# Kernel optimization log

Hardware: AMD Instinct MI355X
Metric: run time of the kernel (lower is better)

## Reference

```python
import jax, jax.numpy as jnp
import numpy as np

# dims: B batch, S seq, IN input, H lstm hidden, OUT output, N memory_size, W memory_width
B, S, IN, H, OUT, N, W = 128, 32, 512, 1024, 512, 16384, 128
C = OUT + W + (2 * W + 3)  # controller_output_size = 899


def setup_inputs() -> dict:
    key = jax.random.key(0)
    ks = jax.random.split(key, 16)
    def p(k, shape, s=0.02):
        return jax.random.normal(k, shape, jnp.float32) * s
    return {
        'x': jax.random.normal(ks[0], (B, S, IN), jnp.float32),
        'memory': p(ks[1], (N, W), 0.1),
        'Wih': p(ks[2], (4 * H, IN + W)), 'Whh': p(ks[3], (4 * H, H)),
        'bih': jnp.zeros(4 * H, jnp.float32), 'bhh': jnp.zeros(4 * H, jnp.float32),
        'Wout': p(ks[4], (C, H)), 'bout': jnp.zeros(C, jnp.float32),
        'rkW': p(ks[5], (W, C)), 'rkb': jnp.zeros(W, jnp.float32),
        'rbW': p(ks[6], (1, C)), 'rbb': jnp.zeros(1, jnp.float32),
        'rgW': p(ks[7], (1, C)), 'rgb': jnp.zeros(1, jnp.float32),
        'wkW': p(ks[8], (W, C)), 'wkb': jnp.zeros(W, jnp.float32),
        'wbW': p(ks[9], (1, C)), 'wbb': jnp.zeros(1, jnp.float32),
        'wgW': p(ks[10], (1, C)), 'wgb': jnp.zeros(1, jnp.float32),
        'erW': p(ks[11], (W, C)), 'erb': jnp.zeros(W, jnp.float32),
        'adW': p(ks[12], (W, C)), 'adb': jnp.zeros(W, jnp.float32),
        'pW': p(ks[13], (OUT, OUT)), 'pb': jnp.zeros(OUT, jnp.float32),
    }


def _l2norm(v, axis):
    n = jnp.linalg.norm(v, axis=axis, keepdims=True)
    return v / jnp.maximum(n, 1e-12)


def reference(x, memory, Wih, Whh, bih, bhh, Wout, bout,
              rkW, rkb, rbW, rbb, rgW, rgb,
              wkW, wkb, wbW, wbb, wgW, wgb,
              erW, erb, adW, adb, pW, pb):
    Bq, Sq, _ = x.shape
    Nq, Wq = memory.shape
    Hq = Whh.shape[1]
    out_size = pW.shape[0]
    sp = jax.nn.softplus
    uniform = jnp.full((Bq, Nq), 1.0 / Nq, x.dtype)

    def addressing(keyv, beta, gamma, prev_w, mem):
        # cosine similarity -> softmax(beta*sim) -> interpolation with prev weights
        sim = _l2norm(keyv, 1) @ _l2norm(mem, 1).T        # [B, N]
        w = jax.nn.softmax(beta * sim, axis=1)
        return gamma * w + (1 - gamma) * prev_w

    def step(carry, xt):
        mem, h, c, prev_rw, prev_rv = carry
        ci = jnp.concatenate([xt, prev_rv], axis=1)       # [B, IN+W]
        g = ci @ Wih.T + h @ Whh.T + bih + bhh
        i_, f_, gg, o_ = jnp.split(g, 4, axis=1)          # torch LSTM gate order i,f,g,o
        c = jax.nn.sigmoid(f_) * c + jax.nn.sigmoid(i_) * jnp.tanh(gg)
        h = jax.nn.sigmoid(o_) * jnp.tanh(c)
        co = h @ Wout.T + bout                            # controller output [B, C]
        # read head
        rkey = co @ rkW.T + rkb
        rbeta = sp(co @ rbW.T + rbb)
        rgamma = 1 + sp(co @ rgW.T + rgb)
        rw = addressing(rkey, rbeta, rgamma, prev_rw, mem)
        # write head (prev weights = uniform, per source)
        wkey = co @ wkW.T + wkb
        wbeta = sp(co @ wbW.T + wbb)
        wgamma = 1 + sp(co @ wgW.T + wgb)
        ww = addressing(wkey, wbeta, wgamma, uniform, mem)
        er = jax.nn.sigmoid(co @ erW.T + erb)             # [B, W]
        ad = jnp.tanh(co @ adW.T + adb)                   # [B, W]
        # MemoryBank.write sums erase/add terms over batch (shared global memory)
        erase = jnp.einsum('bn,bw->nw', ww, er)
        addt = jnp.einsum('bn,bw->nw', ww, ad)
        mem = mem * (1 - erase) + addt
        rv = rw @ mem                                     # read after write [B, W]
        out = co[:, :out_size] @ pW.T + pb
        return (mem, h, c, rw, rv), out

    init = (memory,
            jnp.zeros((Bq, Hq), x.dtype), jnp.zeros((Bq, Hq), x.dtype),
            uniform, jnp.zeros((Bq, Wq), x.dtype))
    _, outs = jax.lax.scan(step, init, jnp.swapaxes(x, 0, 1))
    return jnp.swapaxes(outs, 0, 1)                       # [B, S, OUT]
```

## Files before the change

### kernel.cpp

```cpp
#include <hip/hip_runtime.h>

typedef __attribute__((ext_vector_type(8))) short bf16x8;
typedef __attribute__((ext_vector_type(4))) float f32x4;

__device__ __forceinline__ float bf2f(unsigned short u) {
  union { float f; unsigned int i; } v; v.i = ((unsigned int)u) << 16; return v.f;
}
__device__ __forceinline__ unsigned short f2bf(float f) {
  union { float f; unsigned int i; } v; v.f = f;
  unsigned int r = v.i + 0x7fffu + ((v.i >> 16) & 1u);
  return (unsigned short)(r >> 16);
}
__device__ __forceinline__ float sigf(float x) { return 1.0f / (1.0f + expf(-x)); }
__device__ __forceinline__ float softplusf(float x) {
  return (x > 20.0f) ? x : log1pf(expf(x));
}
__device__ __forceinline__ float sat(float v) {
  return fminf(fmaxf(v, -1.0e6f), 1.0e6f);
}
__device__ __forceinline__ float ldx(const void* p, int is32, long i) {
  return is32 ? ((const float*)p)[i] : bf2f(((const unsigned short*)p)[i]);
}
template<int A32>
__device__ __forceinline__ bf16x8 load8(const void* base, long off) {
  if (A32) {
    const float* p = (const float*)base + off;
    f32x4 a = *(const f32x4*)p;
    f32x4 b = *(const f32x4*)(p + 4);
    bf16x8 r;
    r[0] = (short)f2bf(a[0]); r[1] = (short)f2bf(a[1]);
    r[2] = (short)f2bf(a[2]); r[3] = (short)f2bf(a[3]);
    r[4] = (short)f2bf(b[0]); r[5] = (short)f2bf(b[1]);
    r[6] = (short)f2bf(b[2]); r[7] = (short)f2bf(b[3]);
    return r;
  }
  return *(const bf16x8*)((const unsigned short*)base + off);
}


__global__ __launch_bounds__(64) void probe_dtype(
    const unsigned int* __restrict__ w, int* __restrict__ flags)
{
  const int lane = threadIdx.x;
  int cnt = 0;
  for (int i = 0; i < 16; ++i) {
    unsigned int word = w[lane * 16 + i];
    float av = fabsf(bf2f((unsigned short)(word & 0xFFFFu)));
    if (av > 1.0e-4f && av < 1.0f) cnt++;
  }
  #pragma unroll
  for (int off = 32; off > 0; off >>= 1) cnt += __shfl_xor(cnt, off);
  if (lane == 0) flags[1] = (cnt > 512) ? 0 : 1;
}

__global__ __launch_bounds__(64) void probe_layout(int* __restrict__ flags) {
  const int lane = threadIdx.x;
  const int qr = lane & 15, quad = lane >> 4;
  bf16x8 a, b;
  #pragma unroll
  for (int j = 0; j < 8; ++j) {
    int k = quad * 8 + j;
    a[j] = (short)f2bf((k == qr) ? 1.0f : 0.0f);
    b[j] = (short)f2bf((float)(k + 1));
  }
  f32x4 acc = {0.0f, 0.0f, 0.0f, 0.0f};
  acc = __builtin_amdgcn_mfma_f32_16x16x32_bf16(a, b, acc, 0, 0, 0);
  bool ok0 = true, ok1 = true;
  #pragma unroll
  for (int rg = 0; rg < 4; ++rg) {
    ok0 = ok0 && (acc[rg] == (float)(quad * 4 + rg + 1));
    ok1 = ok1 && (acc[rg] == (float)(qr + 1));
  }
  int a0 = __all(ok0 ? 1 : 0);
  int a1 = __all(ok1 ? 1 : 0);
  if (lane == 0) flags[0] = a0 ? 0 : (a1 ? 1 : 0);
}

template<int BM, int BN, int EPI, int A32, int BT>
__global__ __launch_bounds__(256) void gemm_pipe(
    const void* __restrict__ A, int lda,
    const unsigned short* __restrict__ B, int ldb,
    int kChunk, int Mtot, int Ntot,
    float* __restrict__ C, long long ldc, unsigned short* __restrict__ Cb,
    const int* __restrict__ flags)
{
  constexpr int LDT = 72;
  constexpr int AI = BM / 32;
  constexpr int BI = BN / 32;
  __shared__ unsigned short smem[2][(BM + BN) * LDT];
  const int tid = threadIdx.x;
  const int lane = tid & 63, wid = tid >> 6;
  const int wm = wid & 1, wn = wid >> 1;
  constexpr int WM = BM / 2, WN = BN / 2;
  constexpr int TM = WM / 16, TN = WN / 16;
  const int m0 = blockIdx.x * BM, n0 = blockIdx.y * BN;
  const int kBeg = blockIdx.z * kChunk;
  const int qr = lane & 15, quad = lane >> 4;
  const int NIT = kChunk >> 6;

  f32x4 acc[TM][TN] = {};
  bf16x8 ar[AI], br[BI];

  auto loadAB = [&](int k0) {
    #pragma unroll
    for (int i = 0; i < AI; ++i) {
      int lin = i * 256 + tid; int row = lin >> 3, q = (lin & 7) << 3;
      ar[i] = load8<A32>(A, (long)(m0 + row) * lda + k0 + q);
    }
    #pragma unroll
    for (int i = 0; i < BI; ++i) {
      int lin = i * 256 + tid;
      if (BT) {
        int kl = lin >> 3, nq = (lin & 7) << 3;
        br[i] = *(const bf16x8*)(B + (long)(k0 + kl) * ldb + n0 + nq);
      } else {
        int row = lin >> 3, q = (lin & 7) << 3;
        br[i] = *(const bf16x8*)(B + (long)(n0 + row) * ldb + k0 + q);
      }
    }
  };
  auto stage = [&](int buf) {
    #pragma unroll
    for (int i = 0; i < AI; ++i) {
      int lin = i * 256 + tid; int row = lin >> 3, q = (lin & 7) << 3;
      *(bf16x8*)&smem[buf][row * LDT + q] = ar[i];
    }
    #pragma unroll
    for (int i = 0; i < BI; ++i) {
      int lin = i * 256 + tid;
      if (BT) {
        int kl = lin >> 3, nq = (lin & 7) << 3;
        #pragma unroll
        for (int j = 0; j < 8; ++j)
          smem[buf][(BM + nq + j) * LDT + kl] = (unsigned short)br[i][j];
      } else {
        int row = lin >> 3, q = (lin & 7) << 3;
        *(bf16x8*)&smem[buf][(BM + row) * LDT + q] = br[i];
      }
    }
  };

  loadAB(kBeg);
  stage(0);
  __syncthreads();
  for (int it = 0; it < NIT; ++it) {
    if (it + 1 < NIT) loadAB(kBeg + (it + 1) * 64);
    const unsigned short* As = &smem[it & 1][0];
    const unsigned short* Bs = &smem[it & 1][BM * LDT];
    #pragma unroll
    for (int ks = 0; ks < 64; ks += 32) {
      bf16x8 af[TM], bfv[TN];
      #pragma unroll
      for (int mt = 0; mt < TM; ++mt)
        af[mt] = *(const bf16x8*)&As[(wm * WM + mt * 16 + qr) * LDT + ks + quad * 8];
      #pragma unroll
      for (int nt = 0; nt < TN; ++nt)
        bfv[nt] = *(const bf16x8*)&Bs[(wn * WN + nt * 16 + qr) * LDT + ks + quad * 8];
      #pragma unroll
      for (int mt = 0; mt < TM; ++mt)
        #pragma unroll
        for (int nt = 0; nt < TN; ++nt)
          acc[mt][nt] = __builtin_amdgcn_mfma_f32_16x16x32_bf16(af[mt], bfv[nt], acc[mt][nt], 0, 0, 0);
    }
    if (it + 1 < NIT) { stage((it + 1) & 1); __syncthreads(); }
  }

  const int swap = flags[0];
  #pragma unroll
  for (int mt = 0; mt < TM; ++mt)
    #pragma unroll
    for (int nt = 0; nt < TN; ++nt)
      #pragma unroll
      for (int rg = 0; rg < 4; ++rg) {
        int ri = swap ? qr : (quad * 4 + rg);
        int ci = swap ? (quad * 4 + rg) : qr;
        int gm = m0 + wm * WM + mt * 16 + ri;
        int gn = n0 + wn * WN + nt * 16 + ci;
        float v = sat(acc[mt][nt][rg]);
        if (EPI == 2) Cb[(size_t)gm * ldc + gn] = f2bf(v);
        else C[(size_t)blockIdx.z * Mtot * Ntot + (size_t)gm * Ntot + gn] = v;
      }
}

__global__ __launch_bounds__(256) void gemm_gates(
    const unsigned short* __restrict__ A, const unsigned short* __restrict__ B,
    const float* __restrict__ bsum2, float* __restrict__ c,
    unsigned short* __restrict__ nxt, const unsigned short* __restrict__ x_bf,
    int t, const int* __restrict__ flags)
{
  constexpr int LDT = 72;
  __shared__ unsigned short smem[2][128 * LDT];
  __shared__ float Ssc[64][65];
  const int tid = threadIdx.x;
  const int lane = tid & 63, wid = tid >> 6;
  const int wm = wid & 1, wn = wid >> 1;
  const int m0 = blockIdx.x * 64, n0 = blockIdx.y * 64;
  const int qr = lane & 15, quad = lane >> 4;
  const int NIT = 26;

  f32x4 acc[2][2] = {};
  bf16x8 ar[2], br[2];
  auto loadAB = [&](int k0) {
    #pragma unroll
    for (int i = 0; i < 2; ++i) {
      int lin = i * 256 + tid; int row = lin >> 3, q = (lin & 7) << 3;
      ar[i] = *(const bf16x8*)(A + (long)(m0 + row) * 1664 + k0 + q);
      br[i] = *(const bf16x8*)(B + (long)(n0 + row) * 1664 + k0 + q);
    }
  };
  auto stage = [&](int buf) {
    #pragma unroll
    for (int i = 0; i < 2; ++i) {
      int lin = i * 256 + tid; int row = lin >> 3, q = (lin & 7) << 3;
      *(bf16x8*)&smem[buf][row * LDT + q] = ar[i];
      *(bf16x8*)&smem[buf][(64 + row) * LDT + q] = br[i];
    }
  };
  loadAB(0); stage(0); __syncthreads();
  for (int it = 0; it < NIT; ++it) {
    if (it + 1 < NIT) loadAB((it + 1) * 64);
    const unsigned short* As = &smem[it & 1][0];
    const unsigned short* Bs = &smem[it & 1][64 * LDT];
    #pragma unroll
    for (int ks = 0; ks < 64; ks += 32) {
      bf16x8 af[2], bfv[2];
      #pragma unroll
      for (int mt = 0; mt < 2; ++mt)
        af[mt] = *(const bf16x8*)&As[(wm * 32 + mt * 16 + qr) * LDT + ks + quad * 8];
      #pragma unroll
      for (int nt = 0; nt < 2; ++nt)
        bfv[nt] = *(const bf16x8*)&Bs[(wn * 32 + nt * 16 + qr) * LDT + ks + quad * 8];
      #pragma unroll
      for (int mt = 0; mt < 2; ++mt)
        #pragma unroll
        for (int nt = 0; nt < 2; ++nt)
          acc[mt][nt] = __builtin_amdgcn_mfma_f32_16x16x32_bf16(af[mt], bfv[nt], acc[mt][nt], 0, 0, 0);
    }
    if (it + 1 < NIT) { stage((it + 1) & 1); __syncthreads(); }
  }

  const int swap = flags[0];
  #pragma unroll
  for (int mt = 0; mt < 2; ++mt)
    #pragma unroll
    for (int nt = 0; nt < 2; ++nt)
      #pragma unroll
      for (int rg = 0; rg < 4; ++rg) {
        int ri = swap ? qr : (quad * 4 + rg);
        int ci = swap ? (quad * 4 + rg) : qr;
        Ssc[wn * 32 + nt * 16 + ci][wm * 32 + mt * 16 + ri] = acc[mt][nt][rg];
      }
  __syncthreads();
  {
    const int jl = tid & 15, bh = tid >> 4;
    const int jg = (n0 >> 2) + jl;
    const float b0 = bsum2[n0 + jl * 4 + 0];
    const float b1 = bsum2[n0 + jl * 4 + 1];
    const float b2 = bsum2[n0 + jl * 4 + 2];
    const float b3 = bsum2[n0 + jl * 4 + 3];
    #pragma unroll
    for (int p = 0; p < 4; ++p) {
      int bl = bh + p * 16;
      int bb = m0 + bl;
      float gi_ = Ssc[jl * 4 + 0][bl] + b0;
      float gf  = Ssc[jl * 4 + 1][bl] + b1;
      float gg  = Ssc[jl * 4 + 2][bl] + b2;
      float go  = Ssc[jl * 4 + 3][bl] + b3;
      size_t cix = (size_t)bb * 1024 + jg;
      float cn = sat(sigf(gf) * c[cix] + sigf(gi_) * tanhf(gg));
      c[cix] = cn;
      nxt[bb * 1664 + 640 + jg] = f2bf(sigf(go) * tanhf(cn));
    }
  }
  if (t + 1 < 32) {
    int blk = blockIdx.y * 2 + blockIdx.x;
    #pragma unroll
    for (int i = 0; i < 2; ++i) {
      int e = blk * 512 + i * 256 + tid;
      nxt[(e >> 9) * 1664 + (e & 511)] = x_bf[(size_t)(t + 1) * 65536 + e];
    }
  }
}

__global__ __launch_bounds__(256) void gemm_heads(
    const unsigned short* __restrict__ Wcomb,
    const unsigned short* __restrict__ h, int ldb,
    const float* __restrict__ vcat,
    unsigned short* __restrict__ keys_n, unsigned short* __restrict__ EA,
    float* __restrict__ sc, void* __restrict__ outp, int t,
    const int* __restrict__ flags)
{
  constexpr int BM = 128, BN = 64, LDT = 72;
  __shared__ unsigned short smem[2][(BM + BN) * LDT];
  __shared__ float colss[64];
  __shared__ float cinv[64];
  const int tid = threadIdx.x;
  const int lane = tid & 63, wid = tid >> 6;
  const int wm = wid & 1, wn = wid >> 1;
  constexpr int TM = 4, TN = 2;
  const int m0 = blockIdx.x * BM, n0 = blockIdx.y * BN;
  const int qr = lane & 15, quad = lane >> 4;
  const int NIT = 16;

  f32x4 acc[TM][TN] = {};
  bf16x8 ar[4], br[2];
  auto loadAB = [&](int k0) {
    #pragma unroll
    for (int i = 0; i < 4; ++i) {
      int lin = i * 256 + tid; int row = lin >> 3, q = (lin & 7) << 3;
      ar[i] = *(const bf16x8*)(Wcomb + (long)(m0 + row) * 1024 + k0 + q);
    }
    #pragma unroll
    for (int i = 0; i < 2; ++i) {
      int lin = i * 256 + tid; int row = lin >> 3, q = (lin & 7) << 3;
      br[i] = *(const bf16x8*)(h + (long)(n0 + row) * ldb + k0 + q);
    }
  };
  auto stage = [&](int buf) {
    #pragma unroll
    for (int i = 0; i < 4; ++i) {
      int lin = i * 256 + tid; int row = lin >> 3, q = (lin & 7) << 3;
      *(bf16x8*)&smem[buf][row * LDT + q] = ar[i];
    }
    #pragma unroll
    for (int i = 0; i < 2; ++i) {
      int lin = i * 256 + tid; int row = lin >> 3, q = (lin & 7) << 3;
      *(bf16x8*)&smem[buf][(BM + row) * LDT + q] = br[i];
    }
  };

  loadAB(0);
  stage(0);
  __syncthreads();
  for (int it = 0; it < NIT; ++it) {
    if (it + 1 < NIT) loadAB((it + 1) * 64);
    const unsigned short* As = &smem[it & 1][0];
    const unsigned short* Bs = &smem[it & 1][BM * LDT];
    #pragma unroll
    for (int ks = 0; ks < 64; ks += 32) {
      bf16x8 af[TM], bfv[TN];
      #pragma unroll
      for (int mt = 0; mt < TM; ++mt)
        af[mt] = *(const bf16x8*)&smem[it & 1][(wm * 64 + mt * 16 + qr) * LDT + ks + quad * 8];
      #pragma unroll
      for (int nt = 0; nt < TN; ++nt)
        bfv[nt] = *(const bf16x8*)&Bs[(wn * 32 + nt * 16 + qr) * LDT + ks + quad * 8];
      (void)As;
      #pragma unroll
      for (int mt = 0; mt < TM; ++mt)
        #pragma unroll
        for (int nt = 0; nt < TN; ++nt)
          acc[mt][nt] = __builtin_amdgcn_mfma_f32_16x16x32_bf16(af[mt], bfv[nt], acc[mt][nt], 0, 0, 0);
    }
    if (it + 1 < NIT) { stage((it + 1) & 1); __syncthreads(); }
  }

  const int swap = flags[0];
  const int F = flags[1];
  #pragma unroll
  for (int mt = 0; mt < TM; ++mt)
    #pragma unroll
    for (int nt = 0; nt < TN; ++nt)
      #pragma unroll
      for (int rg = 0; rg < 4; ++rg) {
        int ri = swap ? qr : (quad * 4 + rg);
        int gm = m0 + wm * 64 + mt * 16 + ri;
        acc[mt][nt][rg] = sat(acc[mt][nt][rg] + vcat[gm]);
      }

  if (m0 < 256) {
    if (tid < 64) colss[tid] = 0.0f;
    __syncthreads();
    #pragma unroll
    for (int nt = 0; nt < TN; ++nt)
      #pragma unroll
      for (int rg = 0; rg < 4; ++rg) {
        float part = 0.0f;
        #pragma unroll
        for (int mt = 0; mt < TM; ++mt) {
          float v = acc[mt][nt][rg]; part += v * v;
        }
        int ci = swap ? (quad * 4 + rg) : qr;
        atomicAdd(&colss[wn * 32 + nt * 16 + ci], part);
      }
    __syncthreads();
    if (tid < 64) cinv[tid] = 1.0f / fmaxf(sqrtf(colss[tid]), 1e-12f);
    __syncthreads();
    const int head = m0 >> 7;
    #pragma unroll
    for (int mt = 0; mt < TM; ++mt)
      #pragma unroll
      for (int nt = 0; nt < TN; ++nt)
        #pragma unroll
        for (int rg = 0; rg < 4; ++rg) {
          int ri = swap ? qr : (quad * 4 + rg);
          int ci = swap ? (quad * 4 + rg) : qr;
          int w = wm * 64 + mt * 16 + ri;
          int cl = wn * 32 + nt * 16 + ci;
          keys_n[(size_t)(head * 128 + n0 + cl) * 128 + w] =
              f2bf(acc[mt][nt][rg] * cinv[cl]);
        }
  } else {
    #pragma unroll
    for (int mt = 0; mt < TM; ++mt)
      #pragma unroll
      for (int nt = 0; nt < TN; ++nt)
        #pragma unroll
        for (int rg = 0; rg < 4; ++rg) {
          int ri = swap ? qr : (quad * 4 + rg);
          int ci = swap ? (quad * 4 + rg) : qr;
          int gm = m0 + wm * 64 + mt * 16 + ri;
          int gn = n0 + wn * 32 + nt * 16 + ci;
          float v = acc[mt][nt][rg];
          if (m0 == 256) {
            EA[(size_t)((gm - 256) * 2) * 128 + gn] = f2bf(sigf(v));
          } else if (m0 == 384) {
            EA[(size_t)((gm - 384) * 2 + 1) * 128 + gn] = f2bf(tanhf(v));
          } else if (m0 < 1024) {
            int o = gm - 512;
            size_t idx = (size_t)gn * 16384 + (size_t)t * 512 + o;
            if (F) ((float*)outp)[idx] = v;
            else ((unsigned short*)outp)[idx] = f2bf(v);
          } else if (gm < 1028) {
            float sp = fminf(softplusf(v), 1.0e4f);
            int j = gm - 1024;
            sc[j * 128 + gn] = (j & 1) ? (1.0f + sp) : sp;
          }
        }
  }
}

__global__ __launch_bounds__(256) void softmax1(
    const unsigned short* __restrict__ Csim, const float* __restrict__ sc,
    float* __restrict__ rw, unsigned short* __restrict__ ww)
{
  const int r = blockIdx.x, tid = threadIdx.x;
  const int b = r & 127;
  const bool isRead = r < 128;
  const float beta  = isRead ? sc[b]       : sc[256 + b];
  const float gamma = isRead ? sc[128 + b] : sc[384 + b];
  const unsigned short* row = Csim + (size_t)r * 16384;
  __shared__ float red[4];
  float v[64];
  #pragma unroll
  for (int p = 0; p < 8; ++p) {
    bf16x8 x = *(const bf16x8*)(row + p * 2048 + tid * 8);
    #pragma unroll
    for (int j = 0; j < 8; ++j) v[p * 8 + j] = bf2f((unsigned short)x[j]);
  }
  float mx = -3.0e38f;
  #pragma unroll
  for (int p = 0; p < 64; ++p) mx = fmaxf(mx, v[p]);
  #pragma unroll
  for (int off = 32; off > 0; off >>= 1) mx = fmaxf(mx, __shfl_xor(mx, off));
  if ((tid & 63) == 0) red[tid >> 6] = mx;
  __syncthreads();
  mx = fmaxf(fmaxf(red[0], red[1]), fmaxf(red[2], red[3]));
  const float m = beta * mx;
  __syncthreads();
  float s = 0.0f;
  #pragma unroll
  for (int p = 0; p < 64; ++p) { v[p] = expf(beta * v[p] - m); s += v[p]; }
  #pragma unroll
  for (int off = 32; off > 0; off >>= 1) s += __shfl_xor(s, off);
  if ((tid & 63) == 0) red[tid >> 6] = s;
  __syncthreads();
  s = red[0] + red[1] + red[2] + red[3];
  const float inv = 1.0f / fmaxf(s, 1e-30f);
  if (isRead) {
    float* prow = rw + (size_t)b * 16384;
    #pragma unroll
    for (int p = 0; p < 8; ++p) {
      long base = p * 2048 + tid * 8;
      f32x4 o0 = *(const f32x4*)(prow + base);
      f32x4 o1 = *(const f32x4*)(prow + base + 4);
      #pragma unroll
      for (int j = 0; j < 4; ++j) {
        o0[j] = sat(gamma * v[p * 8 + j] * inv + (1.0f - gamma) * o0[j]);
        o1[j] = sat(gamma * v[p * 8 + 4 + j] * inv + (1.0f - gamma) * o1[j]);
      }
      *(f32x4*)(prow + base) = o0;
      *(f32x4*)(prow + base + 4) = o1;
    }
  } else {
    unsigned short* wrow = ww + (size_t)b * 16384;
    const float u = 1.0f / 16384.0f;
    #pragma unroll
    for (int p = 0; p < 8; ++p) {
      long base = p * 2048 + tid * 8;
      bf16x8 o;
      #pragma unroll
      for (int j = 0; j < 8; ++j)
        o[j] = (short)f2bf(sat(gamma * v[p * 8 + j] * inv + (1.0f - gamma) * u));
      *(bf16x8*)(wrow + base) = o;
    }
  }
}

__global__ __launch_bounds__(256) void write_mem(
    const unsigned short* __restrict__ ww, const unsigned short* __restrict__ EA,
    float* __restrict__ mem, unsigned short* __restrict__ memn,
    unsigned short* __restrict__ mem_bf, const int* __restrict__ flags)
{
  constexpr int LDT = 72;
  __shared__ unsigned short smem[320 * LDT];
  const int tid = threadIdx.x;
  const int lane = tid & 63, wid = tid >> 6;
  const int qr = lane & 15, quad = lane >> 4;
  const int n0 = blockIdx.x * 64;
  f32x4 acc[4][4] = {};
  bf16x8 pa[2], pb[8];

  auto loadRegs = [&](int kk) {
    #pragma unroll
    for (int i = 0; i < 2; ++i) {
      int ch = i * 256 + tid; int bl = ch >> 3, nq = (ch & 7) << 3;
      pa[i] = *(const bf16x8*)(ww + (size_t)(kk * 64 + bl) * 16384 + n0 + nq);
    }
    #pragma unroll
    for (int i = 0; i < 8; ++i) {
      int ch = i * 256 + tid; int j = ch >> 3, q = (ch & 7) << 3;
      pb[i] = *(const bf16x8*)(EA + (size_t)j * 128 + kk * 64 + q);
    }
  };
  auto stageRegs = [&]() {
    #pragma unroll
    for (int i = 0; i < 2; ++i) {
      int ch = i * 256 + tid; int bl = ch >> 3, nq = (ch & 7) << 3;
      #pragma unroll
      for (int j = 0; j < 8; ++j)
        smem[(nq + j) * LDT + bl] = (unsigned short)pa[i][j];
    }
    #pragma unroll
    for (int i = 0; i < 8; ++i) {
      int ch = i * 256 + tid; int j = ch >> 3, q = (ch & 7) << 3;
      *(bf16x8*)&smem[(64 + j) * LDT + q] = pb[i];
    }
  };
  auto doMfma = [&]() {
    #pragma unroll
    for (int ks = 0; ks < 64; ks += 32) {
      bf16x8 af[4], bfv[4];
      #pragma unroll
      for (int mt = 0; mt < 4; ++mt)
        af[mt] = *(const bf16x8*)&smem[(mt * 16 + qr) * LDT + ks + quad * 8];
      #pragma unroll
      for (int nt = 0; nt < 4; ++nt)
        bfv[nt] = *(const bf16x8*)&smem[(64 + wid * 64 + nt * 16 + qr) * LDT + ks + quad * 8];
      #pragma unroll
      for (int mt = 0; mt < 4; ++mt)
        #pragma unroll
        for (int nt = 0; nt < 4; ++nt)
          acc[mt][nt] = __builtin_amdgcn_mfma_f32_16x16x32_bf16(af[mt], bfv[nt], acc[mt][nt], 0, 0, 0);
    }
  };

  loadRegs(0);
  stageRegs();
  loadRegs(1);
  __syncthreads();
  doMfma();
  __syncthreads();
  stageRegs();
  __syncthreads();
  doMfma();
  __syncthreads();

  const int swap = flags[0];
  #pragma unroll
  for (int mt = 0; mt < 4; ++mt)
    #pragma unroll
    for (int nt = 0; nt < 4; ++nt)
      #pragma unroll
      for (int rg = 0; rg < 4; ++rg) {
        int ri = swap ? qr : (quad * 4 + rg);
        int ci = swap ? (quad * 4 + rg) : qr;
        int nl = mt * 16 + ri;
        int j  = wid * 64 + nt * 16 + ci;
        smem[nl * 264 + j] = f2bf(sat(acc[mt][nt][rg]));
      }
  __syncthreads();
  {
    const int nl = tid >> 2, ws = (tid & 3) << 5;
    const unsigned int* Srow = (const unsigned int*)&smem[nl * 264];
    const size_t gbase = (size_t)(n0 + nl) * 128 + ws;
    float nv[32];
    float ss = 0.0f;
    #pragma unroll
    for (int i = 0; i < 32; ++i) {
      unsigned int pr = Srow[ws + i];
      float er = bf2f((unsigned short)(pr & 0xFFFFu));
      float ad = bf2f((unsigned short)(pr >> 16));
      float x = sat(mem[gbase + i] * (1.0f - er) + ad);
      nv[i] = x;
      ss += x * x;
    }
    ss += __shfl_xor(ss, 1);
    ss += __shfl_xor(ss, 2);
    const float inv = 1.0f / fmaxf(sqrtf(ss), 1e-12f);
    #pragma unroll
    for (int i = 0; i < 32; ++i) {
      mem[gbase + i] = nv[i];
      memn[gbase + i] = f2bf(nv[i] * inv);
      mem_bf[gbase + i] = f2bf(nv[i]);
    }
  }
}

__global__ __launch_bounds__(256) void init_mem(
    const void* __restrict__ memory, float* __restrict__ mem,
    unsigned short* __restrict__ memn, unsigned short* __restrict__ mem_bf,
    const int* __restrict__ flags)
{
  const int F = flags[1];
  __shared__ float tile[64][129];
  __shared__ float inv[64];
  const int n0 = blockIdx.x * 64, tid = threadIdx.x;
  for (int e = tid; e < 8192; e += 256) {
    int r = e >> 7, w = e & 127;
    size_t gi = (size_t)(n0 + r) * 128 + w;
    float nv = ldx(memory, F, (long)gi);
    mem[gi] = nv;
    tile[r][w] = nv;
  }
  __syncthreads();
  if (tid < 64) {
    float ss = 0.0f;
    for (int w = 0; w < 128; ++w) { float v = tile[tid][w]; ss += v * v; }
    inv[tid] = 1.0f / fmaxf(sqrtf(ss), 1e-12f);
  }
  __syncthreads();
  for (int e = tid; e < 8192; e += 256) {
    int r = e >> 7, w = e & 127;
    size_t gi = (size_t)(n0 + r) * 128 + w;
    memn[gi] = f2bf(tile[r][w] * inv[r]);
    mem_bf[gi] = f2bf(tile[r][w]);
  }
}

__global__ __launch_bounds__(256) void rv_reduce(
    const float* __restrict__ part, unsigned short* __restrict__ nxt)
{
  int e = blockIdx.x * 256 + threadIdx.x;
  float s = 0.0f;
  for (int z = 0; z < 64; ++z) s += part[(size_t)z * 16384 + e];
  int b = e >> 7, w = e & 127;
  nxt[b * 1664 + 512 + w] = f2bf(sat(s));
}

__global__ void init_pack(
    const void* __restrict__ x, const void* __restrict__ Wih,
    const void* __restrict__ Whh, const void* __restrict__ bih,
    const void* __restrict__ bhh,
    const void* __restrict__ rkW, const void* __restrict__ wkW,
    const void* __restrict__ erW, const void* __restrict__ adW,
    const void* __restrict__ pW,
    const void* __restrict__ rbW, const void* __restrict__ rgW,
    const void* __restrict__ wbW, const void* __restrict__ wgW,
    unsigned short* __restrict__ W_lstm, float* __restrict__ bsum,
    unsigned short* __restrict__ x_bf, unsigned short* __restrict__ Wcat,
    unsigned short* __restrict__ ci_h, float* __restrict__ c,
    float* __restrict__ rw, const int* __restrict__ flags)
{
  const int F = flags[1];
  const long T0 = 4096L * 1664;
  const long T1 = 4096;
  const long T2 = 32L * 128 * 512;
  const long T3 = 1152L * 960;
  const long T4 = 128L * 1664;
  const long T5 = 128L * 1024;
  const long T6 = 128L * 16384;
  const long total = T0 + T1 + T2 + T3 + T4 + T5 + T6;
  for (long e = (long)blockIdx.x * 256 + threadIdx.x; e < total;
       e += (long)gridDim.x * 256) {
    long r = e;
    if (r < T0) {
      int jp = (int)(r / 1664), k = (int)(r % 1664);
      int orow = (jp & 3) * 1024 + (jp >> 2);
      float v = (k < 640) ? ldx(Wih, F, (long)orow * 640 + k)
                          : ldx(Whh, F, (long)orow * 1024 + (k - 640));
      W_lstm[r] = f2bf(v);
      continue;
    }
    r -= T0;
    if (r < T1) {
      long o = (long)(r & 3) * 1024 + (r >> 2);
      bsum[r] = ldx(bih, F, o) + ldx(bhh, F, o);
      continue;
    }
    r -= T1;
    if (r < T2) {
      int t = (int)(r >> 16); long rr = r & 65535;
      int b = (int)(rr >> 9), k = (int)(rr & 511);
      x_bf[r] = f2bf(ldx(x, F, (long)b * 16384 + (long)t * 512 + k));
      continue;
    }
    r -= T2;
    if (r < T3) {
      int j = (int)(r / 960), o = (int)(r % 960);
      float v = 0.0f;
      if (j < 512) {
        if (o < 899) {
          if (j < 128) v = ldx(rkW, F, (long)j * 899 + o);
          else if (j < 256) v = ldx(wkW, F, (long)(j - 128) * 899 + o);
          else if (j < 384) v = ldx(erW, F, (long)(j - 256) * 899 + o);
          else v = ldx(adW, F, (long)(j - 384) * 899 + o);
        }
      } else if (j < 1024) {
        if (o < 512) v = ldx(pW, F, (long)(j - 512) * 512 + o);
      } else if (j < 1028) {
        if (o < 899) {
          const void* s = (j == 1024) ? rbW : (j == 1025) ? rgW
                        : (j == 1026) ? wbW : wgW;
          v = ldx(s, F, o);
        }
      }
      Wcat[r] = f2bf(v);
      continue;
    }
    r -= T3;
    if (r < T4) {
      int b = (int)(r / 1664), k = (int)(r % 1664);
      ci_h[r] = (k < 512) ? f2bf(ldx(x, F, (long)b * 16384 + k)) : (unsigned short)0;
      continue;
    }
    r -= T4;
    if (r < T5) { c[r] = 0.0f; continue; }
    r -= T5;
    rw[r] = 1.0f / 16384.0f;
  }
}

__global__ __launch_bounds__(256) void transpose_wout(
    const void* __restrict__ Wout, unsigned short* __restrict__ WoutT,
    const int* __restrict__ flags)
{
  const int F = flags[1];
  __shared__ float tile[64][65];
  const int n0 = blockIdx.x * 64, o0 = blockIdx.y * 64;
  for (int e = threadIdx.x; e < 4096; e += 256) {
    int ro = e >> 6, cn = e & 63;
    int o = o0 + ro;
    tile[ro][cn] = (o < 899) ? ldx(Wout, F, (long)o * 1024 + n0 + cn) : 0.0f;
  }
  __syncthreads();
  for (int e = threadIdx.x; e < 4096; e += 256) {
    int rn = e >> 6, co = e & 63;
    WoutT[(size_t)(n0 + rn) * 960 + o0 + co] = f2bf(tile[co][rn]);
  }
}

__global__ __launch_bounds__(64) void init_vcat(
    const void* __restrict__ rkW, const void* __restrict__ wkW,
    const void* __restrict__ erW, const void* __restrict__ adW,
    const void* __restrict__ pW,
    const void* __restrict__ rbW, const void* __restrict__ rgW,
    const void* __restrict__ wbW, const void* __restrict__ wgW,
    const void* __restrict__ bout,
    const void* __restrict__ rkb, const void* __restrict__ wkb,
    const void* __restrict__ erb, const void* __restrict__ adb,
    const void* __restrict__ pb,
    const void* __restrict__ rbb, const void* __restrict__ rgb,
    const void* __restrict__ wbb, const void* __restrict__ wgb,
    float* __restrict__ vcat, const int* __restrict__ flags)
{
  const int F = flags[1];
  const int j = blockIdx.x, lane = threadIdx.x;
  if (j >= 1028) { if (lane == 0) vcat[j] = 0.0f; return; }
  const int Kj = (j >= 512 && j < 1024) ? 512 : 899;
  float s = 0.0f;
  for (int o = lane; o < Kj; o += 64) {
    float w;
    if (j < 128) w = ldx(rkW, F, (long)j * 899 + o);
    else if (j < 256) w = ldx(wkW, F, (long)(j - 128) * 899 + o);
    else if (j < 384) w = ldx(erW, F, (long)(j - 256) * 899 + o);
    else if (j < 512) w = ldx(adW, F, (long)(j - 384) * 899 + o);
    else if (j < 1024) w = ldx(pW, F, (long)(j - 512) * 512 + o);
    else {
      const void* sp = (j == 1024) ? rbW : (j == 1025) ? rgW
                     : (j == 1026) ? wbW : wgW;
      w = ldx(sp, F, o);
    }
    s += w * ldx(bout, F, o);
  }
  #pragma unroll
  for (int off = 32; off > 0; off >>= 1) s += __shfl_down(s, off);
  if (lane == 0) {
    float b;
    if (j < 128) b = ldx(rkb, F, j);
    else if (j < 256) b = ldx(wkb, F, j - 128);
    else if (j < 384) b = ldx(erb, F, j - 256);
    else if (j < 512) b = ldx(adb, F, j - 384);
    else if (j < 1024) b = ldx(pb, F, j - 512);
    else if (j == 1024) b = ldx(rbb, F, 0);
    else if (j == 1025) b = ldx(rgb, F, 0);
    else if (j == 1026) b = ldx(wbb, F, 0);
    else b = ldx(wgb, F, 0);
    vcat[j] = s + b;
  }
}

extern "C" void kernel_launch(void* const* d_in, const int* in_sizes, int n_in,
                              void* d_out, int out_size, void* d_ws, size_t ws_size,
                              hipStream_t stream) {
  const void* x      = d_in[0];
  const void* memory = d_in[1];
  const void* Wih    = d_in[2];
  const void* Whh    = d_in[3];
  const void* bih    = d_in[4];
  const void* bhh    = d_in[5];
  const void* Wout   = d_in[6];
  const void* bout   = d_in[7];
  const void* rkW    = d_in[8];
  const void* rkb    = d_in[9];
  const void* rbW    = d_in[10];
  const void* rbb    = d_in[11];
  const void* rgW    = d_in[12];
  const void* rgb    = d_in[13];
  const void* wkW    = d_in[14];
  const void* wkb    = d_in[15];
  const void* wbW    = d_in[16];
  const void* wbb    = d_in[17];
  const void* wgW    = d_in[18];
  const void* wgb    = d_in[19];
  const void* erW    = d_in[20];
  const void* erb    = d_in[21];
  const void* adW    = d_in[22];
  const void* adb    = d_in[23];
  const void* pW     = d_in[24];
  const void* pb     = d_in[25];

  char* p = (char*)d_ws;
  auto alloc = [&](size_t bytes) -> char* {
    char* r = p; p += (bytes + 255) & ~(size_t)255; return r;
  };
  char*           big    = alloc(256L * 16384 * 2);
  unsigned short* Wcat   = (unsigned short*)big;
  unsigned short* WoutT  = (unsigned short*)(big + 2359296);
  unsigned short* W_lstm = (unsigned short*)alloc(4096L * 1664 * 2);
  unsigned short* Wcomb  = (unsigned short*)alloc(1152L * 1024 * 2);
  float*          vcat   = (float*)alloc(1152L * 4);
  float*          bsum   = (float*)alloc(4096L * 4);
  unsigned short* x_bf   = (unsigned short*)alloc(32L * 128 * 512 * 2);
  unsigned short* ci_hA  = (unsigned short*)alloc(128L * 1664 * 2);
  unsigned short* ci_hB  = (unsigned short*)alloc(128L * 1664 * 2);
  float*          c      = (float*)alloc(128L * 1024 * 4);
  unsigned short* keys_n = (unsigned short*)alloc(256L * 128 * 2);
  unsigned short* EA     = (unsigned short*)alloc(256L * 128 * 2);
  float*          sc     = (float*)alloc(4L * 128 * 4);
  float*          rw     = (float*)alloc(128L * 16384 * 4);
  unsigned short* ww_nat = (unsigned short*)alloc(128L * 16384 * 2);
  float*          mem    = (float*)alloc(16384L * 128 * 4);
  unsigned short* memn   = (unsigned short*)alloc(16384L * 128 * 2);
  unsigned short* mem_bf = (unsigned short*)alloc(16384L * 128 * 2);
  int*            flags  = (int*)alloc(256);

  probe_dtype<<<1, 64, 0, stream>>>((const unsigned int*)Whh, flags);
  probe_layout<<<1, 64, 0, stream>>>(flags);
  init_pack<<<8192, 256, 0, stream>>>(x, Wih, Whh, bih, bhh, rkW, wkW, erW, adW,
                                      pW, rbW, rgW, wbW, wgW, W_lstm, bsum, x_bf,
                                      Wcat, ci_hA, c, rw, flags);
  init_mem<<<256, 256, 0, stream>>>(memory, mem, memn, mem_bf, flags);
  transpose_wout<<<dim3(16, 15, 1), 256, 0, stream>>>(Wout, WoutT, flags);
  init_vcat<<<1152, 64, 0, stream>>>(rkW, wkW, erW, adW, pW, rbW, rgW, wbW, wgW,
                                     bout, rkb, wkb, erb, adb, pb, rbb, rgb,
                                     wbb, wgb, vcat, flags);
  gemm_pipe<128, 64, 2, 0, 0><<<dim3(9, 16, 1), 256, 0, stream>>>(
      Wcat, 960, WoutT, 960, 960, 1152, 1024, nullptr, 1024, Wcomb, flags);

  unsigned short* bufs[2] = {ci_hA, ci_hB};
  for (int t = 0; t < 32; ++t) {
    unsigned short* cur = bufs[t & 1];
    unsigned short* nxt = bufs[(t + 1) & 1];
    gemm_gates<<<dim3(2, 64, 1), 256, 0, stream>>>(
        cur, W_lstm, bsum, c, nxt, x_bf, t, flags);
    gemm_heads<<<dim3(9, 2, 1), 256, 0, stream>>>(
        Wcomb, nxt + 640, 1664, vcat, keys_n, EA, sc, d_out, t, flags);
    gemm_pipe<128, 64, 2, 0, 0><<<dim3(2, 256, 1), 256, 0, stream>>>(
        keys_n, 128, memn, 128, 128, 256, 16384, nullptr, 16384,
        (unsigned short*)big, flags);
    softmax1<<<256, 256, 0, stream>>>((const unsigned short*)big, sc, rw, ww_nat);
    write_mem<<<256, 256, 0, stream>>>(ww_nat, EA, mem, memn, mem_bf, flags);
    gemm_pipe<128, 64, 3, 1, 1><<<dim3(1, 2, 64), 256, 0, stream>>>(
        rw, 16384, mem_bf, 128, 256, 128, 128, (float*)big, 128, nullptr, flags);
    rv_reduce<<<64, 256, 0, stream>>>((const float*)big, nxt);
  }
}
```

Baseline: 2.886 ms.

## Replace split-K partial buffer and rv_reduce with atomic accumulation into rv

```diff
diff --git a/kernel.cpp b/kernel.cpp
--- a/kernel.cpp
+++ b/kernel.cpp
@@ -21,18 +21,19 @@
 __device__ __forceinline__ float ldx(const void* p, int is32, long i) {
   return is32 ? ((const float*)p)[i] : bf2f(((const unsigned short*)p)[i]);
 }
+__device__ __forceinline__ bf16x8 packbf(f32x4 a, f32x4 b) {
+  bf16x8 r;
+  r[0] = (short)f2bf(a[0]); r[1] = (short)f2bf(a[1]);
+  r[2] = (short)f2bf(a[2]); r[3] = (short)f2bf(a[3]);
+  r[4] = (short)f2bf(b[0]); r[5] = (short)f2bf(b[1]);
+  r[6] = (short)f2bf(b[2]); r[7] = (short)f2bf(b[3]);
+  return r;
+}
 template<int A32>
 __device__ __forceinline__ bf16x8 load8(const void* base, long off) {
   if (A32) {
     const float* p = (const float*)base + off;
-    f32x4 a = *(const f32x4*)p;
-    f32x4 b = *(const f32x4*)(p + 4);
-    bf16x8 r;
-    r[0] = (short)f2bf(a[0]); r[1] = (short)f2bf(a[1]);
-    r[2] = (short)f2bf(a[2]); r[3] = (short)f2bf(a[3]);
-    r[4] = (short)f2bf(b[0]); r[5] = (short)f2bf(b[1]);
-    r[6] = (short)f2bf(b[2]); r[7] = (short)f2bf(b[3]);
-    return r;
+    return packbf(*(const f32x4*)p, *(const f32x4*)(p + 4));
   }
   return *(const bf16x8*)((const unsigned short*)base + off);
 }
@@ -140,9 +141,7 @@
     }
   };
 
-  loadAB(kBeg);
-  stage(0);
-  __syncthreads();
+  loadAB(kBeg); stage(0); __syncthreads();
   for (int it = 0; it < NIT; ++it) {
     if (it + 1 < NIT) loadAB(kBeg + (it + 1) * 64);
     const unsigned short* As = &smem[it & 1][0];
@@ -176,17 +175,16 @@
         int ci = swap ? (quad * 4 + rg) : qr;
         int gm = m0 + wm * WM + mt * 16 + ri;
         int gn = n0 + wn * WN + nt * 16 + ci;
-        float v = sat(acc[mt][nt][rg]);
-        if (EPI == 2) Cb[(size_t)gm * ldc + gn] = f2bf(v);
-        else C[(size_t)blockIdx.z * Mtot * Ntot + (size_t)gm * Ntot + gn] = v;
+        if (EPI == 2) Cb[(size_t)gm * ldc + gn] = f2bf(sat(acc[mt][nt][rg]));
+        else atomicAdd(&C[(size_t)gm * ldc + gn], acc[mt][nt][rg]);
       }
 }
 
 __global__ __launch_bounds__(256) void gemm_gates(
-    const unsigned short* __restrict__ A, const unsigned short* __restrict__ B,
+    const unsigned short* __restrict__ h, const float* __restrict__ rvf,
+    const unsigned short* __restrict__ x_bf, const unsigned short* __restrict__ B,
     const float* __restrict__ bsum2, float* __restrict__ c,
-    unsigned short* __restrict__ nxt, const unsigned short* __restrict__ x_bf,
-    int t, const int* __restrict__ flags)
+    unsigned short* __restrict__ hnxt, int t, const int* __restrict__ flags)
 {
   constexpr int LDT = 72;
   __shared__ unsigned short smem[2][128 * LDT];
@@ -204,7 +202,15 @@
     #pragma unroll
     for (int i = 0; i < 2; ++i) {
       int lin = i * 256 + tid; int row = lin >> 3, q = (lin & 7) << 3;
-      ar[i] = *(const bf16x8*)(A + (long)(m0 + row) * 1664 + k0 + q);
+      int gb = m0 + row;
+      if (k0 < 512) {
+        ar[i] = *(const bf16x8*)(x_bf + (size_t)t * 65536 + (size_t)gb * 512 + k0 + q);
+      } else if (k0 < 640) {
+        const float* pp = rvf + (size_t)gb * 128 + (k0 - 512) + q;
+        ar[i] = packbf(*(const f32x4*)pp, *(const f32x4*)(pp + 4));
+      } else {
+        ar[i] = *(const bf16x8*)(h + (size_t)gb * 1024 + (k0 - 640) + q);
+      }
       br[i] = *(const bf16x8*)(B + (long)(n0 + row) * 1664 + k0 + q);
     }
   };
@@ -269,22 +275,14 @@
       size_t cix = (size_t)bb * 1024 + jg;
       float cn = sat(sigf(gf) * c[cix] + sigf(gi_) * tanhf(gg));
       c[cix] = cn;
-      nxt[bb * 1664 + 640 + jg] = f2bf(sigf(go) * tanhf(cn));
-    }
-  }
-  if (t + 1 < 32) {
-    int blk = blockIdx.y * 2 + blockIdx.x;
-    #pragma unroll
-    for (int i = 0; i < 2; ++i) {
-      int e = blk * 512 + i * 256 + tid;
-      nxt[(e >> 9) * 1664 + (e & 511)] = x_bf[(size_t)(t + 1) * 65536 + e];
+      hnxt[(size_t)bb * 1024 + jg] = f2bf(sigf(go) * tanhf(cn));
     }
   }
 }
 
 __global__ __launch_bounds__(256) void gemm_heads(
     const unsigned short* __restrict__ Wcomb,
-    const unsigned short* __restrict__ h, int ldb,
+    const unsigned short* __restrict__ h,
     const float* __restrict__ vcat,
     unsigned short* __restrict__ keys_n, unsigned short* __restrict__ EA,
     float* __restrict__ sc, void* __restrict__ outp, int t,
@@ -313,7 +311,7 @@
     #pragma unroll
     for (int i = 0; i < 2; ++i) {
       int lin = i * 256 + tid; int row = lin >> 3, q = (lin & 7) << 3;
-      br[i] = *(const bf16x8*)(h + (long)(n0 + row) * ldb + k0 + q);
+      br[i] = *(const bf16x8*)(h + (long)(n0 + row) * 1024 + k0 + q);
     }
   };
   auto stage = [&](int buf) {
@@ -329,12 +327,9 @@
     }
   };
 
-  loadAB(0);
-  stage(0);
-  __syncthreads();
+  loadAB(0); stage(0); __syncthreads();
   for (int it = 0; it < NIT; ++it) {
     if (it + 1 < NIT) loadAB((it + 1) * 64);
-    const unsigned short* As = &smem[it & 1][0];
     const unsigned short* Bs = &smem[it & 1][BM * LDT];
     #pragma unroll
     for (int ks = 0; ks < 64; ks += 32) {
@@ -345,7 +340,6 @@
       #pragma unroll
       for (int nt = 0; nt < TN; ++nt)
         bfv[nt] = *(const bf16x8*)&Bs[(wn * 32 + nt * 16 + qr) * LDT + ks + quad * 8];
-      (void)As;
       #pragma unroll
       for (int mt = 0; mt < TM; ++mt)
         #pragma unroll
@@ -377,9 +371,7 @@
       for (int rg = 0; rg < 4; ++rg) {
         float part = 0.0f;
         #pragma unroll
-        for (int mt = 0; mt < TM; ++mt) {
-          float v = acc[mt][nt][rg]; part += v * v;
-        }
+        for (int mt = 0; mt < TM; ++mt) { float v = acc[mt][nt][rg]; part += v * v; }
         int ci = swap ? (quad * 4 + rg) : qr;
         atomicAdd(&colss[wn * 32 + nt * 16 + ci], part);
       }
@@ -397,8 +389,7 @@
           int ci = swap ? (quad * 4 + rg) : qr;
           int w = wm * 64 + mt * 16 + ri;
           int cl = wn * 32 + nt * 16 + ci;
-          keys_n[(size_t)(head * 128 + n0 + cl) * 128 + w] =
-              f2bf(acc[mt][nt][rg] * cinv[cl]);
+          keys_n[(size_t)(head * 128 + n0 + cl) * 128 + w] = f2bf(acc[mt][nt][rg] * cinv[cl]);
         }
   } else {
     #pragma unroll
@@ -432,7 +423,8 @@
 
 __global__ __launch_bounds__(256) void softmax1(
     const unsigned short* __restrict__ Csim, const float* __restrict__ sc,
-    float* __restrict__ rw, unsigned short* __restrict__ ww)
+    float* __restrict__ rw, unsigned short* __restrict__ ww,
+    float* __restrict__ rvf)
 {
   const int r = blockIdx.x, tid = threadIdx.x;
   const int b = r & 127;
@@ -441,6 +433,7 @@
   const float gamma = isRead ? sc[128 + b] : sc[384 + b];
   const unsigned short* row = Csim + (size_t)r * 16384;
   __shared__ float red[4];
+  if (tid < 64) rvf[r * 64 + tid] = 0.0f;
   float v[64];
   #pragma unroll
   for (int p = 0; p < 8; ++p) {
@@ -510,7 +503,6 @@
   const int n0 = blockIdx.x * 64;
   f32x4 acc[4][4] = {};
   bf16x8 pa[2], pb[8];
-
   auto loadRegs = [&](int kk) {
     #pragma unroll
     for (int i = 0; i < 2; ++i) {
@@ -554,18 +546,9 @@
           acc[mt][nt] = __builtin_amdgcn_mfma_f32_16x16x32_bf16(af[mt], bfv[nt], acc[mt][nt], 0, 0, 0);
     }
   };
-
-  loadRegs(0);
-  stageRegs();
-  loadRegs(1);
-  __syncthreads();
-  doMfma();
-  __syncthreads();
-  stageRegs();
-  __syncthreads();
-  doMfma();
-  __syncthreads();
-
+  loadRegs(0); stageRegs(); loadRegs(1);
+  __syncthreads(); doMfma(); __syncthreads();
+  stageRegs(); __syncthreads(); doMfma(); __syncthreads();
   const int swap = flags[0];
   #pragma unroll
   for (int mt = 0; mt < 4; ++mt)
@@ -575,9 +558,7 @@
       for (int rg = 0; rg < 4; ++rg) {
         int ri = swap ? qr : (quad * 4 + rg);
         int ci = swap ? (quad * 4 + rg) : qr;
-        int nl = mt * 16 + ri;
-        int j  = wid * 64 + nt * 16 + ci;
-        smem[nl * 264 + j] = f2bf(sat(acc[mt][nt][rg]));
+        smem[(mt * 16 + ri) * 264 + wid * 64 + nt * 16 + ci] = f2bf(sat(acc[mt][nt][rg]));
       }
   __syncthreads();
   {
@@ -636,16 +617,6 @@
     memn[gi] = f2bf(tile[r][w] * inv[r]);
     mem_bf[gi] = f2bf(tile[r][w]);
   }
-}
-
-__global__ __launch_bounds__(256) void rv_reduce(
-    const float* __restrict__ part, unsigned short* __restrict__ nxt)
-{
-  int e = blockIdx.x * 256 + threadIdx.x;
-  float s = 0.0f;
-  for (int z = 0; z < 64; ++z) s += part[(size_t)z * 16384 + e];
-  int b = e >> 7, w = e & 127;
-  nxt[b * 1664 + 512 + w] = f2bf(sat(s));
 }
 
 __global__ void init_pack(
@@ -659,18 +630,20 @@
     const void* __restrict__ wbW, const void* __restrict__ wgW,
     unsigned short* __restrict__ W_lstm, float* __restrict__ bsum,
     unsigned short* __restrict__ x_bf, unsigned short* __restrict__ Wcat,
-    unsigned short* __restrict__ ci_h, float* __restrict__ c,
-    float* __restrict__ rw, const int* __restrict__ flags)
+    float* __restrict__ c, float* __restrict__ rw,
+    unsigned short* __restrict__ hA, float* __restrict__ rvf,
+    const int* __restrict__ flags)
 {
   const int F = flags[1];
   const long T0 = 4096L * 1664;
   const long T1 = 4096;
   const long T2 = 32L * 128 * 512;
   const long T3 = 1152L * 960;
-  const long T4 = 128L * 1664;
-  const long T5 = 128L * 1024;
-  const long T6 = 128L * 16384;
-  const long total = T0 + T1 + T2 + T3 + T4 + T5 + T6;
+  const long T4 = 128L * 1024;
+  const long T5 = 128L * 16384;
+  const long T6 = 128L * 1024;
+  const long T7 = 128L * 128;
+  const long total = T0 + T1 + T2 + T3 + T4 + T5 + T6 + T7;
   for (long e = (long)blockIdx.x * 256 + threadIdx.x; e < total;
        e += (long)gridDim.x * 256) {
     long r = e;
@@ -719,15 +692,13 @@
       continue;
     }
     r -= T3;
-    if (r < T4) {
-      int b = (int)(r / 1664), k = (int)(r % 1664);
-      ci_h[r] = (k < 512) ? f2bf(ldx(x, F, (long)b * 16384 + k)) : (unsigned short)0;
-      continue;
-    }
+    if (r < T4) { c[r] = 0.0f; continue; }
     r -= T4;
-    if (r < T5) { c[r] = 0.0f; continue; }
+    if (r < T5) { rw[r] = 1.0f / 16384.0f; continue; }
     r -= T5;
-    rw[r] = 1.0f / 16384.0f;
+    if (r < T6) { hA[r] = 0; continue; }
+    r -= T6;
+    rvf[r] = 0.0f;
   }
 }
 
@@ -842,9 +813,10 @@
   float*          vcat   = (float*)alloc(1152L * 4);
   float*          bsum   = (float*)alloc(4096L * 4);
   unsigned short* x_bf   = (unsigned short*)alloc(32L * 128 * 512 * 2);
-  unsigned short* ci_hA  = (unsigned short*)alloc(128L * 1664 * 2);
-  unsigned short* ci_hB  = (unsigned short*)alloc(128L * 1664 * 2);
+  unsigned short* hA     = (unsigned short*)alloc(128L * 1024 * 2);
+  unsigned short* hB     = (unsigned short*)alloc(128L * 1024 * 2);
   float*          c      = (float*)alloc(128L * 1024 * 4);
+  float*          rvf    = (float*)alloc(128L * 128 * 4);
   unsigned short* keys_n = (unsigned short*)alloc(256L * 128 * 2);
   unsigned short* EA     = (unsigned short*)alloc(256L * 128 * 2);
   float*          sc     = (float*)alloc(4L * 128 * 4);
@@ -859,7 +831,7 @@
   probe_layout<<<1, 64, 0, stream>>>(flags);
   init_pack<<<8192, 256, 0, stream>>>(x, Wih, Whh, bih, bhh, rkW, wkW, erW, adW,
                                       pW, rbW, rgW, wbW, wgW, W_lstm, bsum, x_bf,
-                                      Wcat, ci_hA, c, rw, flags);
+                                      Wcat, c, rw, hA, rvf, flags);
   init_mem<<<256, 256, 0, stream>>>(memory, mem, memn, mem_bf, flags);
   transpose_wout<<<dim3(16, 15, 1), 256, 0, stream>>>(Wout, WoutT, flags);
   init_vcat<<<1152, 64, 0, stream>>>(rkW, wkW, erW, adW, pW, rbW, rgW, wbW, wgW,
@@ -868,21 +840,20 @@
   gemm_pipe<128, 64, 2, 0, 0><<<dim3(9, 16, 1), 256, 0, stream>>>(
       Wcat, 960, WoutT, 960, 960, 1152, 1024, nullptr, 1024, Wcomb, flags);
 
-  unsigned short* bufs[2] = {ci_hA, ci_hB};
+  unsigned short* hbuf[2] = {hA, hB};
   for (int t = 0; t < 32; ++t) {
-    unsigned short* cur = bufs[t & 1];
-    unsigned short* nxt = bufs[(t + 1) & 1];
+    unsigned short* hcur = hbuf[t & 1];
+    unsigned short* hnxt = hbuf[(t + 1) & 1];
     gemm_gates<<<dim3(2, 64, 1), 256, 0, stream>>>(
-        cur, W_lstm, bsum, c, nxt, x_bf, t, flags);
+        hcur, rvf, x_bf, W_lstm, bsum, c, hnxt, t, flags);
     gemm_heads<<<dim3(9, 2, 1), 256, 0, stream>>>(
-        Wcomb, nxt + 640, 1664, vcat, keys_n, EA, sc, d_out, t, flags);
+        Wcomb, hnxt, vcat, keys_n, EA, sc, d_out, t, flags);
     gemm_pipe<128, 64, 2, 0, 0><<<dim3(2, 256, 1), 256, 0, stream>>>(
         keys_n, 128, memn, 128, 128, 256, 16384, nullptr, 16384,
         (unsigned short*)big, flags);
-    softmax1<<<256, 256, 0, stream>>>((const unsigned short*)big, sc, rw, ww_nat);
+    softmax1<<<256, 256, 0, stream>>>((const unsigned short*)big, sc, rw, ww_nat, rvf);
     write_mem<<<256, 256, 0, stream>>>(ww_nat, EA, mem, memn, mem_bf, flags);
-    gemm_pipe<128, 64, 3, 1, 1><<<dim3(1, 2, 64), 256, 0, stream>>>(
-        rw, 16384, mem_bf, 128, 256, 128, 128, (float*)big, 128, nullptr, flags);
-    rv_reduce<<<64, 256, 0, stream>>>((const float*)big, nxt);
-  }
-}
+    gemm_pipe<128, 64, 4, 1, 1><<<dim3(1, 2, 32), 256, 0, stream>>>(
+        rw, 16384, mem_bf, 128, 512, 128, 128, rvf, 128, nullptr, flags);
+  }
+}
```

After: 3.057 ms. +5.9%, slower.
